# Kernel optimization log

Measured on AMD Instinct MI355X. Metric: run time of the kernel, lower is better.

Reference implementation:

```python
import jax, jax.numpy as jnp
import numpy as np

HIDDEN = 1024
NUM_HEADS = 16
BATCH = 2
SEQ = 2048


def setup_inputs() -> dict:
    key = jax.random.key(0)
    ks = jax.random.split(key, 5)
    scale = 1.0 / np.sqrt(HIDDEN)
    return {
        "x": jax.random.normal(ks[0], (BATCH, SEQ, HIDDEN), dtype=jnp.float32),
        "W_qkv": jax.random.normal(ks[1], (HIDDEN, 3 * HIDDEN), dtype=jnp.float32) * scale,
        "b_qkv": jax.random.normal(ks[2], (3 * HIDDEN,), dtype=jnp.float32) * 0.02,
        "W_o": jax.random.normal(ks[3], (HIDDEN, HIDDEN), dtype=jnp.float32) * scale,
        "b_o": jax.random.normal(ks[4], (HIDDEN,), dtype=jnp.float32) * 0.02,
    }


def reference(x, W_qkv, b_qkv, W_o, b_o):
    # x: [B, S, H]
    B, S, H = x.shape
    nh = NUM_HEADS
    hs = H // nh
    qkv = jnp.einsum('bsh,hk->bsk', x, W_qkv) + b_qkv  # [B, S, 3H]
    Q, K, V = qkv[..., :H], qkv[..., H:2 * H], qkv[..., 2 * H:]
    # split heads: [B, nh, S, hs]
    Q = Q.reshape(B, S, nh, hs).transpose(0, 2, 1, 3)
    K = K.reshape(B, S, nh, hs).transpose(0, 2, 1, 3)
    V = V.reshape(B, S, nh, hs).transpose(0, 2, 1, 3)
    scores = jnp.einsum('bnqd,bnkd->bnqk', Q, K) / jnp.sqrt(jnp.asarray(hs, x.dtype))
    # NOTE: the original module applies no causal mask despite its name.
    probs = jax.nn.softmax(scores, axis=-1)
    av = jnp.einsum('bnqk,bnkd->bqnd', probs, V)  # [B, S, nh, hs]
    av = av.reshape(B, S, H)
    return jnp.einsum('bsh,ho->bso', av, W_o) + b_o
```

## Files before the change

kernel.cpp:

```cpp
#include <hip/hip_runtime.h>
#include <hip/hip_bf16.h>
#include <stdint.h>

#define HIDDEN 1024
#define NHEAD  16
#define HS     64
#define BATCH  2
#define SEQ    2048
#define MTOT   (BATCH*SEQ)
#define NQKV   (3*HIDDEN)

typedef __hip_bfloat16 bf16;
typedef __attribute__((ext_vector_type(8))) short s16x8;
typedef __attribute__((ext_vector_type(4))) short s16x4;
typedef __attribute__((ext_vector_type(4))) float f32x4;
typedef __attribute__((ext_vector_type(16))) float f32x16;

__device__ __forceinline__ short f2bf(float f) {
  bf16 h = __float2bfloat16(f);
  return *reinterpret_cast<short*>(&h);
}

__device__ __forceinline__ unsigned cvt_pk_bf16(float lo, float hi) {
  unsigned r;
  asm("v_cvt_pk_bf16_f32 %0, %1, %2" : "=v"(r) : "v"(lo), "v"(hi));
  return r;
}

__device__ __forceinline__ int swz(int row, int blk) {
  return (row*8 + (blk ^ (row & 7)))*8;
}

#define GLOAD_LDS(gp, lp) \
  __builtin_amdgcn_global_load_lds((const __attribute__((address_space(1))) void*)(gp), \
                                   (__attribute__((address_space(3))) void*)(lp), 16, 0, 0)

__device__ __forceinline__ int xcd_swz(int orig, int nwg) {
  return (orig & 7)*(nwg >> 3) + (orig >> 3);
}

__global__ void k_cvt_x(const float* __restrict__ x, short* __restrict__ xb, int n8) {
  int i = blockIdx.x*256 + threadIdx.x;
  if (i >= n8) return;
  const f32x4* xv = (const f32x4*)x;
  f32x4 a = xv[2*i], b = xv[2*i+1];
  s16x8 o = { f2bf(a[0]), f2bf(a[1]), f2bf(a[2]), f2bf(a[3]),
              f2bf(b[0]), f2bf(b[1]), f2bf(b[2]), f2bf(b[3]) };
  *(s16x8*)&xb[i*8] = o;
}

__global__ void k_cvt_wT(const float* __restrict__ W, bf16* __restrict__ WT, int K, int N) {
  __shared__ __align__(16) float tile[64][65];
  int n0 = blockIdx.x*64, k0 = blockIdx.y*64;
  int t = threadIdx.x;
  #pragma unroll
  for (int c = 0; c < 4; c++) {
    int s = c*256 + t;
    int r = s >> 4;
    int cc = s & 15;
    f32x4 v = *(const f32x4*)&W[(size_t)(k0 + r)*N + n0 + cc*4];
    tile[r][cc*4+0] = v[0]; tile[r][cc*4+1] = v[1];
    tile[r][cc*4+2] = v[2]; tile[r][cc*4+3] = v[3];
  }
  __syncthreads();
  #pragma unroll
  for (int c = 0; c < 2; c++) {
    int s = c*256 + t;
    int r = s >> 3;
    int cc = s & 7;
    s16x8 o;
    #pragma unroll
    for (int u = 0; u < 8; u++) o[u] = f2bf(tile[cc*8+u][r]);
    *(s16x8*)&WT[(size_t)(n0 + r)*K + k0 + cc*8] = o;
  }
}

template<int OUT_BF16>
__global__ __launch_bounds__(256) void k_gemm(
    const bf16* __restrict__ A, const bf16* __restrict__ BT,
    const float* __restrict__ bias, void* __restrict__ Cout,
    bf16* __restrict__ VtOut,
    int M, int N, int K)
{
  __shared__ __align__(16) short Asl[128*64];
  __shared__ __align__(16) short Bsl[128*64];
  int t = threadIdx.x;
  int lane = t & 63, w = t >> 6;
  int q = lane & 15, g = lane >> 4;
  int nwg = gridDim.x*gridDim.y;
  int swzid = xcd_swz(blockIdx.y*gridDim.x + blockIdx.x, nwg);
  int bx = swzid % gridDim.x, by = swzid / gridDim.x;
  int row0 = by*128, col0 = bx*128;
  int wr = (w >> 1)*64, wc = (w & 1)*64;

  f32x4 acc[4][4] = {};

  for (int kt = 0; kt < K; kt += 64) {
    __syncthreads();
    #pragma unroll
    for (int c = 0; c < 4; c++) {
      int s = c*256 + t, r = s >> 3, bd = s & 7, bs = bd ^ (r & 7);
      GLOAD_LDS(&A[(size_t)(row0 + r)*K + kt + bs*8], &Asl[s*8]);
      GLOAD_LDS(&BT[(size_t)(col0 + r)*K + kt + bs*8], &Bsl[s*8]);
    }
    __syncthreads();
    #pragma unroll
    for (int kk = 0; kk < 2; kk++) {
      s16x8 af[4], bfr[4];
      #pragma unroll
      for (int i = 0; i < 4; i++) {
        af[i]  = *(const s16x8*)&Asl[swz(wr + i*16 + q, kk*4 + g)];
        bfr[i] = *(const s16x8*)&Bsl[swz(wc + i*16 + q, kk*4 + g)];
      }
      __builtin_amdgcn_s_setprio(1);
      #pragma unroll
      for (int i = 0; i < 4; i++)
        #pragma unroll
        for (int j = 0; j < 4; j++)
          acc[i][j] = __builtin_amdgcn_mfma_f32_16x16x32_bf16(af[i], bfr[j], acc[i][j], 0, 0, 0);
      __builtin_amdgcn_s_setprio(0);
    }
  }

  bool vpath = OUT_BF16 && (VtOut != nullptr) && (col0 >= 2*HIDDEN);
  #pragma unroll
  for (int i = 0; i < 4; i++) {
    #pragma unroll
    for (int j = 0; j < 4; j++) {
      int col = col0 + wc + j*16 + q;
      float bv = bias[col];
      int rowb = row0 + wr + i*16 + g*4;
      if (vpath) {
        int d = col & 63;
        int h = (col >> 6) & 15;
        int b = rowb >> 11;
        int s = rowb & (SEQ - 1);
        int sw = (s & ~12) | ((s & 4) << 1) | ((s & 8) >> 1);
        s16x4 pk = { f2bf(acc[i][j][0] + bv), f2bf(acc[i][j][1] + bv),
                     f2bf(acc[i][j][2] + bv), f2bf(acc[i][j][3] + bv) };
        *(s16x4*)&VtOut[((size_t)((b*16 + h)*64 + d))*SEQ + sw] = pk;
      } else {
        #pragma unroll
        for (int r = 0; r < 4; r++) {
          float v = acc[i][j][r] + bv;
          if (OUT_BF16)
            ((bf16*)Cout)[(size_t)(rowb + r)*N + col] = __float2bfloat16(v);
          else
            ((float*)Cout)[(size_t)(rowb + r)*N + col] = v;
        }
      }
    }
  }
}

__device__ __forceinline__ void attn_stage(
    const bf16* __restrict__ kbase, const bf16* __restrict__ vbase,
    int kv, int th, short* Ks, short* Vs)
{
  #pragma unroll
  for (int c = 0; c < 2; c++) {
    int s = c*256 + th, r = s >> 3, bd = s & 7, bs = bd ^ (r & 7);
    GLOAD_LDS(&kbase[(size_t)(kv + r)*NQKV + bs*8], &Ks[s*8]);
  }
  #pragma unroll
  for (int c = 0; c < 2; c++) {
    int s = c*256 + th, d = s >> 3, bd = s & 7, bs = bd ^ (d & 7);
    GLOAD_LDS(&vbase[(size_t)d*SEQ + kv + bs*8], &Vs[s*8]);
  }
}

struct AttnState {
  float psum[2];
  f32x16 oacc[2][2];
};

__device__ __forceinline__ void attn_compute(
    const short* Ks, const short* Vs, const s16x8 qf[2][4],
    int ql, int hi, AttnState& st)
{
  const float SC2 = 0.125f*1.44269504f;
  const float CB  = -12.f*1.44269504f;
  #pragma unroll
  for (int kb = 0; kb < 2; kb++) {
    s16x8 ka[4];
    int krow = kb*32 + ql;
    #pragma unroll
    for (int ks = 0; ks < 4; ks++) {
      int ch = (ks*2 + hi) ^ (krow & 7);
      ka[ks] = *(const s16x8*)&Ks[(krow*8 + ch)*8];
    }
    s16x8 vfrag[2][2];
    #pragma unroll
    for (int kq = 0; kq < 2; kq++) {
      #pragma unroll
      for (int db = 0; db < 2; db++) {
        int row = db*32 + ql;
        int ch = (kb*4 + kq*2 + hi) ^ (row & 7);
        vfrag[kq][db] = *(const s16x8*)&Vs[(row*8 + ch)*8];
      }
    }
    #pragma unroll
    for (int qb = 0; qb < 2; qb++) {
      f32x16 sf = {};
      __builtin_amdgcn_s_setprio(1);
      #pragma unroll
      for (int ks = 0; ks < 4; ks++)
        sf = __builtin_amdgcn_mfma_f32_32x32x16_bf16(ka[ks], qf[qb][ks], sf, 0, 0, 0);
      __builtin_amdgcn_s_setprio(0);

      unsigned pkw[8];
      #pragma unroll
      for (int i = 0; i < 8; i++) {
        float p0 = __builtin_amdgcn_exp2f(__builtin_fmaf(sf[2*i],   SC2, CB));
        float p1 = __builtin_amdgcn_exp2f(__builtin_fmaf(sf[2*i+1], SC2, CB));
        st.psum[qb] += p0 + p1;
        pkw[i] = cvt_pk_bf16(p0, p1);
      }

      __builtin_amdgcn_s_setprio(1);
      #pragma unroll
      for (int kq = 0; kq < 2; kq++) {
        union { unsigned u[4]; s16x8 v; } pu;
        pu.u[0] = pkw[kq*4]; pu.u[1] = pkw[kq*4+1];
        pu.u[2] = pkw[kq*4+2]; pu.u[3] = pkw[kq*4+3];
        s16x8 pa = pu.v;
        #pragma unroll
        for (int db = 0; db < 2; db++)
          st.oacc[qb][db] = __builtin_amdgcn_mfma_f32_32x32x16_bf16(pa, vfrag[kq][db], st.oacc[qb][db], 0, 0, 0);
      }
      __builtin_amdgcn_s_setprio(0);
    }
  }
}

__global__ __launch_bounds__(512) void k_attn(
    const bf16* __restrict__ qkv, const bf16* __restrict__ Vt, bf16* __restrict__ av)
{
  __shared__ __align__(16) short smem[8*4096];
  int t = threadIdx.x;
  int lane = t & 63, w = t >> 6;
  int half = t >> 8, th = t & 255, wq = w & 3;
  int ql = lane & 31, hi = lane >> 5;
  int nwg = gridDim.x*gridDim.y;
  int swzid = xcd_swz(blockIdx.y*gridDim.x + blockIdx.x, nwg);
  int qt = swzid & 7, bh = swzid >> 3;
  int b = bh >> 4, h = bh & 15;

  short* Ks0 = &smem[half*16384];
  short* Vs0 = Ks0 + 4096;
  short* Ks1 = Ks0 + 8192;
  short* Vs1 = Ks0 + 12288;

  s16x8 qf[2][4];
  #pragma unroll
  for (int qb = 0; qb < 2; qb++) {
    const bf16* qrow = qkv + (size_t)(b*SEQ + qt*256 + wq*64 + qb*32 + ql)*NQKV + h*HS;
    #pragma unroll
    for (int ks = 0; ks < 4; ks++)
      qf[qb][ks] = *(const s16x8*)&qrow[ks*16 + hi*8];
  }

  AttnState st;
  st.psum[0] = 0.f; st.psum[1] = 0.f;
  st.oacc[0][0] = (f32x16){}; st.oacc[0][1] = (f32x16){};
  st.oacc[1][0] = (f32x16){}; st.oacc[1][1] = (f32x16){};

  const bf16* kbase = qkv + (size_t)(b*SEQ)*NQKV + HIDDEN + h*HS;
  const bf16* vbase = Vt + (size_t)(bh*HS)*SEQ;
  int kv0 = half*1024;

  attn_stage(kbase, vbase, kv0, th, Ks0, Vs0);
  __syncthreads();

  #pragma unroll 1
  for (int tt = 0; tt < 16; tt += 2) {
    if (tt + 1 < 16) attn_stage(kbase, vbase, kv0 + (tt+1)*64, th, Ks1, Vs1);
    attn_compute(Ks0, Vs0, qf, ql, hi, st);
    __syncthreads();
    if (tt + 2 < 16) attn_stage(kbase, vbase, kv0 + (tt+2)*64, th, Ks0, Vs0);
    attn_compute(Ks1, Vs1, qf, ql, hi, st);
    __syncthreads();
  }

  float* combO = (float*)smem;
  float* combP = (float*)&smem[16384];
  #pragma unroll
  for (int qb = 0; qb < 2; qb++) {
    if (half == 1) {
      #pragma unroll
      for (int db = 0; db < 2; db++)
        #pragma unroll
        for (int r = 0; r < 16; r++)
          combO[((wq*2 + db)*16 + r)*64 + lane] = st.oacc[qb][db][r];
      combP[wq*64 + lane] = st.psum[qb];
    }
    __syncthreads();
    if (half == 0) {
      #pragma unroll
      for (int db = 0; db < 2; db++)
        #pragma unroll
        for (int r = 0; r < 16; r++)
          st.oacc[qb][db][r] += combO[((wq*2 + db)*16 + r)*64 + lane];
      st.psum[qb] += combP[wq*64 + lane];
    }
    __syncthreads();
  }

  if (half == 0) {
    float linv[2];
    #pragma unroll
    for (int qb = 0; qb < 2; qb++) {
      float ps = st.psum[qb] + __shfl_xor(st.psum[qb], 32);
      linv[qb] = 1.f/ps;
    }
    #pragma unroll
    for (int qb = 0; qb < 2; qb++) {
      #pragma unroll
      for (int r = 0; r < 16; r++) {
        int qr = (r & 3) + 8*(r >> 2) + 4*hi;
        float lr = __shfl(linv[qb], qr);
        int row = b*SEQ + qt*256 + wq*64 + qb*32 + qr;
        bf16* orow = av + (size_t)row*HIDDEN + h*HS;
        orow[ql]      = __float2bfloat16(st.oacc[qb][0][r]*lr);
        orow[32 + ql] = __float2bfloat16(st.oacc[qb][1][r]*lr);
      }
    }
  }
}

extern "C" void kernel_launch(void* const* d_in, const int* in_sizes, int n_in,
                              void* d_out, int out_size, void* d_ws, size_t ws_size,
                              hipStream_t stream) {
  const float* x    = (const float*)d_in[0];
  const float* Wqkv = (const float*)d_in[1];
  const float* bqkv = (const float*)d_in[2];
  const float* Wo   = (const float*)d_in[3];
  const float* bo   = (const float*)d_in[4];

  char* ws = (char*)d_ws;
  bf16* xb    = (bf16*)(ws);
  bf16* av    = xb;
  bf16* WqkvT = (bf16*)(ws + (8  << 20));
  bf16* WoT   = (bf16*)(ws + (14 << 20));
  bf16* qkv   = (bf16*)(ws + (16 << 20));
  bf16* Vt    = (bf16*)(ws + (40 << 20));

  k_cvt_x<<<dim3(MTOT*HIDDEN/8/256), 256, 0, stream>>>(x, (short*)xb, MTOT*HIDDEN/8);
  k_cvt_wT<<<dim3(NQKV/64, HIDDEN/64), 256, 0, stream>>>(Wqkv, WqkvT, HIDDEN, NQKV);
  k_cvt_wT<<<dim3(HIDDEN/64, HIDDEN/64), 256, 0, stream>>>(Wo, WoT, HIDDEN, HIDDEN);
  k_gemm<1><<<dim3(NQKV/128, MTOT/128), 256, 0, stream>>>(xb, WqkvT, bqkv, qkv, Vt, MTOT, NQKV, HIDDEN);
  k_attn<<<dim3(SEQ/256, BATCH*NHEAD), 512, 0, stream>>>(qkv, Vt, av);
  k_gemm<0><<<dim3(HIDDEN/128, MTOT/128), 256, 0, stream>>>(av, WoT, bo, d_out, nullptr, MTOT, HIDDEN, HIDDEN);
}
```

Baseline: 108.8 us.

## Double-buffer GEMM LDS tiles with BK=32 and prefetch next tile

```diff
diff --git a/kernel.cpp b/kernel.cpp
--- a/kernel.cpp
+++ b/kernel.cpp
@@ -29,6 +29,9 @@
 
 __device__ __forceinline__ int swz(int row, int blk) {
   return (row*8 + (blk ^ (row & 7)))*8;
+}
+__device__ __forceinline__ int swz4(int row, int blk) {
+  return (row*4 + (blk ^ ((row >> 1) & 3)))*8;
 }
 
 #define GLOAD_LDS(gp, lp) \
@@ -82,8 +85,8 @@
     bf16* __restrict__ VtOut,
     int M, int N, int K)
 {
-  __shared__ __align__(16) short Asl[128*64];
-  __shared__ __align__(16) short Bsl[128*64];
+  __shared__ __align__(16) short Asl[2][128*32];
+  __shared__ __align__(16) short Bsl[2][128*32];
   int t = threadIdx.x;
   int lane = t & 63, w = t >> 6;
   int q = lane & 15, g = lane >> 4;
@@ -94,32 +97,42 @@
   int wr = (w >> 1)*64, wc = (w & 1)*64;
 
   f32x4 acc[4][4] = {};
-
-  for (int kt = 0; kt < K; kt += 64) {
-    __syncthreads();
-    #pragma unroll
-    for (int c = 0; c < 4; c++) {
-      int s = c*256 + t, r = s >> 3, bd = s & 7, bs = bd ^ (r & 7);
-      GLOAD_LDS(&A[(size_t)(row0 + r)*K + kt + bs*8], &Asl[s*8]);
-      GLOAD_LDS(&BT[(size_t)(col0 + r)*K + kt + bs*8], &Bsl[s*8]);
-    }
-    __syncthreads();
-    #pragma unroll
-    for (int kk = 0; kk < 2; kk++) {
-      s16x8 af[4], bfr[4];
-      #pragma unroll
-      for (int i = 0; i < 4; i++) {
-        af[i]  = *(const s16x8*)&Asl[swz(wr + i*16 + q, kk*4 + g)];
-        bfr[i] = *(const s16x8*)&Bsl[swz(wc + i*16 + q, kk*4 + g)];
-      }
-      __builtin_amdgcn_s_setprio(1);
-      #pragma unroll
-      for (int i = 0; i < 4; i++)
-        #pragma unroll
-        for (int j = 0; j < 4; j++)
-          acc[i][j] = __builtin_amdgcn_mfma_f32_16x16x32_bf16(af[i], bfr[j], acc[i][j], 0, 0, 0);
-      __builtin_amdgcn_s_setprio(0);
-    }
+  int nt = K >> 5;
+
+  #pragma unroll
+  for (int c = 0; c < 2; c++) {
+    int s = c*256 + t, r = s >> 2, bd = s & 3, bs = bd ^ ((r >> 1) & 3);
+    GLOAD_LDS(&A[(size_t)(row0 + r)*K + bs*8], &Asl[0][s*8]);
+    GLOAD_LDS(&BT[(size_t)(col0 + r)*K + bs*8], &Bsl[0][s*8]);
+  }
+  __syncthreads();
+
+  int cur = 0;
+  for (int ti = 0; ti < nt; ti++) {
+    if (ti + 1 < nt) {
+      int kt = (ti + 1) << 5;
+      #pragma unroll
+      for (int c = 0; c < 2; c++) {
+        int s = c*256 + t, r = s >> 2, bd = s & 3, bs = bd ^ ((r >> 1) & 3);
+        GLOAD_LDS(&A[(size_t)(row0 + r)*K + kt + bs*8], &Asl[cur^1][s*8]);
+        GLOAD_LDS(&BT[(size_t)(col0 + r)*K + kt + bs*8], &Bsl[cur^1][s*8]);
+      }
+    }
+    s16x8 af[4], bfr[4];
+    #pragma unroll
+    for (int i = 0; i < 4; i++) {
+      af[i]  = *(const s16x8*)&Asl[cur][swz4(wr + i*16 + q, g)];
+      bfr[i] = *(const s16x8*)&Bsl[cur][swz4(wc + i*16 + q, g)];
+    }
+    __builtin_amdgcn_s_setprio(1);
+    #pragma unroll
+    for (int i = 0; i < 4; i++)
+      #pragma unroll
+      for (int j = 0; j < 4; j++)
+        acc[i][j] = __builtin_amdgcn_mfma_f32_16x16x32_bf16(af[i], bfr[j], acc[i][j], 0, 0, 0);
+    __builtin_amdgcn_s_setprio(0);
+    __syncthreads();
+    cur ^= 1;
   }
 
   bool vpath = OUT_BF16 && (VtOut != nullptr) && (col0 >= 2*HIDDEN);
```

After: 115.3 us. +6.0%, slower.
